# Kernel optimization log

Hardware: AMD Instinct MI355X
Metric: run time of the kernel (lower is better)

## Reference

```python
import jax, jax.numpy as jnp
import numpy as np


def conv2d(x, w, pad, groups=1):
    # x: [B,Cin,H,W], w: [Cout,Cin/groups,K,K]
    return jax.lax.conv_general_dilated(
        x, w, (1, 1), [(pad, pad), (pad, pad)],
        dimension_numbers=('NCHW', 'OIHW', 'NCHW'),
        feature_group_count=groups)


def setup_inputs() -> dict:
    key = jax.random.key(0)
    ks = jax.random.split(key, 24)
    B, C, H, W = 16, 512, 32, 128          # batch, encoder_dim, feature map
    Da, Ds, De, Dm = 512, 256, 256, 1024   # att_dim, state_dim, embed_dim, mem_dim
    V, Dmerge = 1000, 512
    K, P = 11, 5
    Din = De + C + Dm                       # GRU input dim = 1792
    s = 0.02
    rn = lambda k, shp, sc=1.0: jax.random.normal(k, shp, jnp.float32) * sc
    return {
        'encode': rn(ks[0], (B, C, H, W)),
        'encode_pro': rn(ks[1], (B, Da, H, W)),
        'encode_mask': jnp.ones((B, 1, H, W), jnp.float32),
        'state': rn(ks[2], (B, Ds)),
        'pre_weight': jax.random.uniform(ks[3], (B, 1, H, W), jnp.float32),
        'cum_weight': jax.random.uniform(ks[4], (B, 1, H, W), jnp.float32),
        'context': rn(ks[5], (B, C)),
        'cond_mem': rn(ks[6], (B, Dm)),
        'cond_weight': jax.random.uniform(ks[7], (B, 2, H, W), jnp.float32),
        'label_id': jax.random.randint(ks[8], (B,), 0, V),
        # ImageAttention params (all bias-free per source)
        'w_wt': rn(ks[9], (Da, 1, K, K), s),
        'w_cwt': rn(ks[10], (Da, 1, K, K), s),
        'w_condwt': rn(ks[11], (2 * Da, 1, K, K), s),   # groups=2
        'w_energy': rn(ks[12], (Da,), s),               # 1x1 conv -> vector
        'w_state': rn(ks[13], (Da, Ds), s),
        'w_ctx': rn(ks[14], (Da, C), s),
        'w_cond': rn(ks[15], (Da, Dm), s),
        # GRU params
        'w_i2s': rn(ks[16], (Ds, Din), s), 'b_i2s': jnp.zeros((Ds,), jnp.float32),
        'w_i2g': rn(ks[17], (2 * Ds, Din), s), 'b_i2g': jnp.zeros((2 * Ds,), jnp.float32),
        'w_s2g': rn(ks[18], (2 * Ds, Ds), s),
        'w_h2h': rn(ks[19], (Ds, Ds), s),
        # Readout params
        'embed_table': rn(ks[20], (V, De), s),
        'w_l1': rn(ks[21], (Dmerge, De + Ds + C), s), 'b_l1': jnp.zeros((Dmerge,), jnp.float32),
        'w_l2': rn(ks[22], (V, Dmerge), s), 'b_l2': jnp.zeros((V,), jnp.float32),
    }


def reference(encode, encode_pro, encode_mask, state, pre_weight, cum_weight,
              context, cond_mem, cond_weight, label_id, w_wt, w_cwt, w_condwt,
              w_energy, w_state, w_ctx, w_cond, w_i2s, b_i2s, w_i2g, b_i2g,
              w_s2g, w_h2h, embed_table, w_l1, b_l1, w_l2, b_l2):
    P = (w_wt.shape[-1] - 1) // 2
    Da = w_energy.shape[0]
    B, C, H, W = encode.shape
    # --- ImageAttention ---
    t_pre = conv2d(pre_weight, w_wt, P)           # [B,Da,H,W]
    t_cum = conv2d(cum_weight, w_cwt, P)          # [B,Da,H,W]
    t_cw = conv2d(cond_weight, w_condwt, P, groups=2)
    t_cw = t_cw.reshape(B, 2, Da, H, W).sum(1)    # [B,Da,H,W]
    st = state @ w_state.T + context @ w_ctx.T + cond_mem @ w_cond.T  # [B,Da]
    concat_info = jnp.tanh(st[:, :, None, None] + t_pre + t_cum + t_cw + encode_pro)
    energies = jnp.einsum('bchw,c->bhw', concat_info, w_energy)
    energies = energies + (encode_mask[:, 0] - 1.0) * 1e8
    att = jax.nn.softmax(energies.reshape(B, H * W), axis=1)
    new_weight = att.reshape(B, 1, H, W)
    new_cum_weight = cum_weight + new_weight
    ctx = jnp.einsum('bchw,bhw->bc', encode, new_weight[:, 0])  # [B,C]
    # --- GRU transition (data = [embed, ctx, cond_mem]) ---
    embed = embed_table[label_id]
    data = jnp.concatenate([embed, ctx, cond_mem], axis=1)
    gate = data @ w_i2g.T + b_i2g + state @ w_s2g.T
    Ds = state.shape[1]
    update_g = jax.nn.sigmoid(gate[:, :Ds])
    reset_g = jax.nn.sigmoid(gate[:, Ds:])
    state_hat = jnp.tanh(data @ w_i2s.T + b_i2s + (state * reset_g) @ w_h2h.T)
    new_state = update_g * state_hat + (1.0 - update_g) * state
    # --- Readout.step ---
    merged = jnp.concatenate([embed, new_state, ctx], axis=1)
    hid = jax.nn.relu(merged @ w_l1.T + b_l1)
    readout = hid @ w_l2.T + b_l2                  # [B,V]
    return readout
```

## Files before the change

kernel.cpp:

```cpp
#include <hip/hip_runtime.h>
#include <math.h>

typedef unsigned short u16;
typedef __bf16 bf16x8 __attribute__((ext_vector_type(8)));
typedef float f32x4 __attribute__((ext_vector_type(4)));

__device__ u16   g_A_pack[16 * 512 * 32];
__device__ float g_st[16 * 512];
__device__ float g_eraw[16 * 4096];
__device__ float g_energ[16 * 4096];
__device__ float g_data[16 * 1792];
__device__ float g_merged[16 * 1024];
__device__ float g_update[16 * 256];
__device__ float g_reset[16 * 256];
__device__ float g_i2s[16 * 256];
__device__ float g_hid[16 * 512];

__device__ __forceinline__ u16 f2bf(float f) {
    unsigned u = __float_as_uint(f);
    u = (u + 0x7FFFu + ((u >> 16) & 1u)) >> 16;
    return (u16)u;
}
__device__ __forceinline__ float bf2f(u16 u) {
    return __uint_as_float(((unsigned)u) << 16);
}
__device__ __forceinline__ float fast_tanh(float x) {
    return 1.0f - 2.0f / (__expf(2.0f * x) + 1.0f);
}
__device__ __forceinline__ float sigmoidf_(float x) {
    return 1.0f / (1.0f + __expf(-x));
}

__global__ void k_pre(const float* __restrict__ w_wt, const float* __restrict__ w_cwt,
                      const float* __restrict__ w_condwt, const float* __restrict__ state,
                      const float* __restrict__ context, const float* __restrict__ cond_mem,
                      const float* __restrict__ w_state, const float* __restrict__ w_ctx,
                      const float* __restrict__ w_cond, const int* __restrict__ label,
                      const float* __restrict__ embed_table) {
    int bid = blockIdx.x;
    if (bid < 1024) {
        int idx = bid * 256 + threadIdx.x;
        int d = idx >> 9, k = idx & 511;
        float f = 0.f;
        if (k < 484) {
            int c = k / 121, rem = k % 121;
            if (c == 0)      f = w_wt[d * 121 + rem];
            else if (c == 1) f = w_cwt[d * 121 + rem];
            else if (c == 2) f = w_condwt[d * 121 + rem];
            else             f = w_condwt[(512 + d) * 121 + rem];
        }
        int ks = k >> 5, kl = k & 31;
        g_A_pack[(ks * 512 + d) * 32 + kl] = f2bf(f);
    } else if (bid < 3072) {
        int wid = ((bid - 1024) * 256 + threadIdx.x) >> 6;
        int lane = threadIdx.x & 63;
        if (wid >= 16 * 512) return;
        int b = wid >> 9, d = wid & 511;
        float acc = 0.f;
        for (int k = lane; k < 256; k += 64)  acc += state[b * 256 + k]    * w_state[d * 256 + k];
        for (int k = lane; k < 512; k += 64)  acc += context[b * 512 + k]  * w_ctx[d * 512 + k];
        for (int k = lane; k < 1024; k += 64) acc += cond_mem[b * 1024 + k] * w_cond[d * 1024 + k];
        for (int off = 32; off; off >>= 1) acc += __shfl_down(acc, off, 64);
        if (lane == 0) g_st[b * 512 + d] = acc;
    } else {
        int b = bid - 3072, tid = threadIdx.x;
        int lbl = label[b];
        float ev = embed_table[lbl * 256 + tid];
        g_data[b * 1792 + tid] = ev;
        g_merged[b * 1024 + tid] = ev;
        for (int k = tid; k < 1024; k += 256)
            g_data[b * 1792 + 768 + k] = cond_mem[b * 1024 + k];
    }
}

__global__ __launch_bounds__(512, 4) void k_conv_energy(
    const float* __restrict__ pre_w, const float* __restrict__ cum_w, const float* __restrict__ cond_w,
    const float* __restrict__ encode_pro, const float* __restrict__ w_energy)
{
    __shared__ __align__(16) u16 src[4][11][76];
    __shared__ __align__(16) u16 bchunk[64][40];
    __shared__ __align__(16) u16 epro_l[512 * 68];

    const int blk = blockIdx.x;
    const int pxh = blk & 1;
    const int h = (blk >> 1) & 31;
    const int b = blk >> 6;
    const int px0 = pxh * 64;

    const int tid = threadIdx.x;
    const int lane = tid & 63, wv = tid >> 6;
    const int lr = lane & 15, lg = lane >> 4;

    const float* epbase = encode_pro + (size_t)b * 512 * 4096 + h * 128 + px0;

#pragma unroll
    for (int it = 0; it < 7; ++it) {
        int t = tid + it * 512;
        if (t < 4 * 11 * 76) {
            int c = t / (11 * 76);
            int rem = t % (11 * 76);
            int i = rem / 76, x = rem % 76;
            int row = h + i - 5, w = px0 - 5 + x;
            u16 v = 0;
            if (x < 74 && row >= 0 && row < 32 && w >= 0 && w < 128) {
                const float* img = (c == 0) ? pre_w + b * 4096
                                 : (c == 1) ? cum_w + b * 4096
                                 : (c == 2) ? cond_w + b * 8192
                                            : cond_w + b * 8192 + 4096;
                v = f2bf(img[row * 128 + w]);
            }
            src[c][i][x] = v;
        }
    }
    __syncthreads();

    const int kl = tid & 31;
    const int n0 = tid >> 5;
#define BUILD(KS)                                                               \
    {                                                                           \
        int kg = (KS) * 32 + kl;                                                \
        int c = 0, i = 0, jj = 0;                                               \
        bool ok = (kg < 484);                                                   \
        if (ok) { c = kg / 121; int r2 = kg % 121; i = r2 / 11; jj = r2 % 11; } \
        _Pragma("unroll")                                                       \
        for (int rep = 0; rep < 4; ++rep) {                                     \
            int n = n0 + rep * 16;                                              \
            bchunk[n][kl] = ok ? src[c][i][n + jj] : (u16)0;                    \
        }                                                                       \
    }

    f32x4 acc[4][4];
#pragma unroll
    for (int mt = 0; mt < 4; ++mt)
#pragma unroll
        for (int nt = 0; nt < 4; ++nt) {
            f32x4 z = {0.f, 0.f, 0.f, 0.f};
            acc[mt][nt] = z;
        }

    BUILD(0);
    __syncthreads();

#pragma unroll
    for (int ks = 0; ks < 16; ++ks) {
        const int o = ks * 2048 + tid * 4;
        const int er = o >> 6, ec = o & 63;
        float4 epv = *reinterpret_cast<const float4*>(&epbase[(size_t)er * 4096 + ec]);

        bf16x8 afr[4];
#pragma unroll
        for (int mt = 0; mt < 4; ++mt) {
            int d = wv * 64 + mt * 16 + lr;
            afr[mt] = *reinterpret_cast<const bf16x8*>(&g_A_pack[(ks * 512 + d) * 32 + lg * 8]);
        }
        bf16x8 bfr[4];
#pragma unroll
        for (int nt = 0; nt < 4; ++nt)
            bfr[nt] = *reinterpret_cast<const bf16x8*>(&bchunk[nt * 16 + lr][lg * 8]);

#pragma unroll
        for (int mt = 0; mt < 4; ++mt)
#pragma unroll
            for (int nt = 0; nt < 4; ++nt)
                acc[mt][nt] = __builtin_amdgcn_mfma_f32_16x16x32_bf16(afr[mt], bfr[nt], acc[mt][nt], 0, 0, 0);

        {
            ushort4 s;
            s.x = f2bf(epv.x); s.y = f2bf(epv.y); s.z = f2bf(epv.z); s.w = f2bf(epv.w);
            *reinterpret_cast<ushort4*>(&epro_l[er * 68 + ec]) = s;
        }

        __syncthreads();
        if (ks < 15) {
            BUILD(ks + 1);
            __syncthreads();
        }
    }
#undef BUILD

    float e[4] = {0.f, 0.f, 0.f, 0.f};
#pragma unroll
    for (int mt = 0; mt < 4; ++mt) {
#pragma unroll
        for (int r = 0; r < 4; ++r) {
            int d = wv * 64 + mt * 16 + lg * 4 + r;
            float stv = g_st[b * 512 + d];
            float wev = w_energy[d];
#pragma unroll
            for (int nt = 0; nt < 4; ++nt) {
                int px = nt * 16 + lr;
                float val = stv + acc[mt][nt][r] + bf2f(epro_l[d * 68 + px]);
                e[nt] += wev * fast_tanh(val);
            }
        }
    }

    float* ered = reinterpret_cast<float*>(&bchunk[0][0]);
    __syncthreads();
#pragma unroll
    for (int nt = 0; nt < 4; ++nt) {
        float v = e[nt];
        v += __shfl_xor(v, 16, 64);
        v += __shfl_xor(v, 32, 64);
        if (lane < 16) ered[wv * 64 + nt * 16 + lane] = v;
    }
    __syncthreads();
    if (tid < 64) {
        float v = 0.f;
#pragma unroll
        for (int w = 0; w < 8; ++w) v += ered[w * 64 + tid];
        g_eraw[b * 4096 + h * 128 + px0 + tid] = v;
    }
}

__global__ void k_softmax(const float* __restrict__ encode_mask) {
    __shared__ float red[256];
    int b = blockIdx.x, tid = threadIdx.x;
    float v[16];
    float mx = -1e30f;
#pragma unroll
    for (int i = 0; i < 16; ++i) {
        int idx = b * 4096 + tid + i * 256;
        float ev = g_eraw[idx] + (encode_mask[idx] - 1.0f) * 1e8f;
        v[i] = ev; mx = fmaxf(mx, ev);
    }
    red[tid] = mx; __syncthreads();
    for (int s = 128; s; s >>= 1) { if (tid < s) red[tid] = fmaxf(red[tid], red[tid + s]); __syncthreads(); }
    mx = red[0]; __syncthreads();
    float sum = 0.f;
#pragma unroll
    for (int i = 0; i < 16; ++i) { v[i] = __expf(v[i] - mx); sum += v[i]; }
    red[tid] = sum; __syncthreads();
    for (int s = 128; s; s >>= 1) { if (tid < s) red[tid] += red[tid + s]; __syncthreads(); }
    float inv = 1.0f / red[0];
#pragma unroll
    for (int i = 0; i < 16; ++i) g_energ[b * 4096 + tid + i * 256] = v[i] * inv;
}

__global__ void k_ctx(const float* __restrict__ encode) {
    int wid = (blockIdx.x * blockDim.x + threadIdx.x) >> 6;
    int lane = threadIdx.x & 63;
    if (wid >= 16 * 512) return;
    int b = wid >> 9, c = wid & 511;
    const float* e = encode + (size_t)wid * 4096;
    const float* a = g_energ + b * 4096;
    float acc = 0.f;
#pragma unroll
    for (int it = 0; it < 16; ++it) {
        int base = it * 256 + lane * 4;
        float4 ev = *reinterpret_cast<const float4*>(&e[base]);
        float4 av = *reinterpret_cast<const float4*>(&a[base]);
        acc += ev.x * av.x + ev.y * av.y + ev.z * av.z + ev.w * av.w;
    }
    for (int off = 32; off; off >>= 1) acc += __shfl_down(acc, off, 64);
    if (lane == 0) { g_data[b * 1792 + 256 + c] = acc; g_merged[b * 1024 + 512 + c] = acc; }
}

__global__ void k_e1(const float* __restrict__ state,
                     const float* __restrict__ w_i2g, const float* __restrict__ b_i2g,
                     const float* __restrict__ w_s2g, const float* __restrict__ w_i2s,
                     const float* __restrict__ b_i2s) {
    int wid = (blockIdx.x * blockDim.x + threadIdx.x) >> 6;
    int lane = threadIdx.x & 63;
    if (wid >= 16 * 768) return;
    int b = wid / 768, o = wid % 768;
    const float* dt = g_data + b * 1792;
    float acc = 0.f;
    if (o < 512) {
        const float* wr = w_i2g + o * 1792;
        for (int k = lane; k < 1792; k += 64) acc += dt[k] * wr[k];
        const float* wsg = w_s2g + o * 256;
        for (int k = lane; k < 256; k += 64) acc += state[b * 256 + k] * wsg[k];
    } else {
        const float* wr = w_i2s + (o - 512) * 1792;
        for (int k = lane; k < 1792; k += 64) acc += dt[k] * wr[k];
    }
    for (int off = 32; off; off >>= 1) acc += __shfl_down(acc, off, 64);
    if (lane == 0) {
        if (o < 256)       g_update[b * 256 + o]        = sigmoidf_(acc + b_i2g[o]);
        else if (o < 512)  g_reset[b * 256 + (o - 256)] = sigmoidf_(acc + b_i2g[o]);
        else               g_i2s[b * 256 + (o - 512)]   = acc + b_i2s[o - 512];
    }
}

__global__ void k_e2(const float* __restrict__ state, const float* __restrict__ w_h2h) {
    int wid = (blockIdx.x * blockDim.x + threadIdx.x) >> 6;
    int lane = threadIdx.x & 63;
    if (wid >= 16 * 256) return;
    int b = wid >> 8, d = wid & 255;
    const float* wr = w_h2h + d * 256;
    float acc = 0.f;
    for (int k = lane; k < 256; k += 64)
        acc += state[b * 256 + k] * g_reset[b * 256 + k] * wr[k];
    for (int off = 32; off; off >>= 1) acc += __shfl_down(acc, off, 64);
    if (lane == 0) {
        float sh = fast_tanh(g_i2s[b * 256 + d] + acc);
        float u = g_update[b * 256 + d];
        g_merged[b * 1024 + 256 + d] = u * sh + (1.f - u) * state[b * 256 + d];
    }
}

__global__ void k_e3(const float* __restrict__ w_l1, const float* __restrict__ b_l1) {
    int wid = (blockIdx.x * blockDim.x + threadIdx.x) >> 6;
    int lane = threadIdx.x & 63;
    if (wid >= 16 * 512) return;
    int b = wid >> 9, m = wid & 511;
    const float* mg = g_merged + b * 1024;
    const float* wr = w_l1 + m * 1024;
    float acc = 0.f;
    for (int k = lane; k < 1024; k += 64) acc += mg[k] * wr[k];
    for (int off = 32; off; off >>= 1) acc += __shfl_down(acc, off, 64);
    if (lane == 0) g_hid[b * 512 + m] = fmaxf(acc + b_l1[m], 0.f);
}

__global__ void k_e4(const float* __restrict__ w_l2, const float* __restrict__ b_l2,
                     float* __restrict__ out) {
    int wid = (blockIdx.x * blockDim.x + threadIdx.x) >> 6;
    int lane = threadIdx.x & 63;
    if (wid >= 16 * 1000) return;
    int b = wid / 1000, v = wid % 1000;
    const float* hd = g_hid + b * 512;
    const float* wr = w_l2 + v * 512;
    float acc = 0.f;
    for (int k = lane; k < 512; k += 64) acc += hd[k] * wr[k];
    for (int off = 32; off; off >>= 1) acc += __shfl_down(acc, off, 64);
    if (lane == 0) out[b * 1000 + v] = acc + b_l2[v];
}

extern "C" void kernel_launch(void* const* d_in, const int* in_sizes, int n_in,
                              void* d_out, int out_size, void* d_ws, size_t ws_size,
                              hipStream_t stream) {
    static const int EXP[28] = {
        33554432, 33554432, 65536, 4096, 65536, 65536, 8192, 16384, 131072, 16,
        61952, 61952, 123904, 512, 131072, 262144, 524288, 458752, 256, 917504,
        512, 131072, 65536, 256000, 524288, 512, 512000, 1000};
    if (n_in != 28) return;
    for (int i = 0; i < 28; ++i)
        if (in_sizes[i] != EXP[i]) return;

    const float* encode      = (const float*)d_in[0];
    const float* encode_pro  = (const float*)d_in[1];
    const float* encode_mask = (const float*)d_in[2];
    const float* state       = (const float*)d_in[3];
    const float* pre_weight  = (const float*)d_in[4];
    const float* cum_weight  = (const float*)d_in[5];
    const float* context     = (const float*)d_in[6];
    const float* cond_mem    = (const float*)d_in[7];
    const float* cond_weight = (const float*)d_in[8];
    const int*   label_id    = (const int*)d_in[9];
    const float* w_wt     = (const float*)d_in[10];
    const float* w_cwt    = (const float*)d_in[11];
    const float* w_condwt = (const float*)d_in[12];
    const float* w_energy = (const float*)d_in[13];
    const float* w_state  = (const float*)d_in[14];
    const float* w_ctx    = (const float*)d_in[15];
    const float* w_cond   = (const float*)d_in[16];
    const float* w_i2s    = (const float*)d_in[17];
    const float* b_i2s    = (const float*)d_in[18];
    const float* w_i2g    = (const float*)d_in[19];
    const float* b_i2g    = (const float*)d_in[20];
    const float* w_s2g    = (const float*)d_in[21];
    const float* w_h2h    = (const float*)d_in[22];
    const float* embed_t  = (const float*)d_in[23];
    const float* w_l1     = (const float*)d_in[24];
    const float* b_l1     = (const float*)d_in[25];
    const float* w_l2     = (const float*)d_in[26];
    const float* b_l2     = (const float*)d_in[27];
    float* out = (float*)d_out;
    (void)d_ws; (void)ws_size;

    k_pre<<<3088, 256, 0, stream>>>(w_wt, w_cwt, w_condwt, state, context, cond_mem,
                                    w_state, w_ctx, w_cond, label_id, embed_t);
    k_conv_energy<<<1024, 512, 0, stream>>>(pre_weight, cum_weight, cond_weight,
                                            encode_pro, w_energy);
    k_softmax<<<16, 256, 0, stream>>>(encode_mask);
    k_ctx<<<2048, 256, 0, stream>>>(encode);
    k_e1<<<3072, 256, 0, stream>>>(state, w_i2g, b_i2g, w_s2g, w_i2s, b_i2s);
    k_e2<<<1024, 256, 0, stream>>>(state, w_h2h);
    k_e3<<<2048, 256, 0, stream>>>(w_l1, b_l1);
    k_e4<<<4000, 256, 0, stream>>>(w_l2, b_l2, out);
}
```

Baseline: 178.8 us.

## Fuse softmax into context kernel and hoist encode_pro staging before MFMA loop

Two changes. The per-batch softmax is folded into the context-reduction kernel: each of 512 blocks recomputes its batch's softmax into shared memory and then reduces 16 channels against it. This removes a kernel launch and the global round trip of the attention weights, at the cost of computing the softmax redundantly 32 times per batch. Separately, the conv-energy kernel now loads and bf16-converts the whole encode_pro tile up front instead of interleaving those loads with the MFMA k-loop, and that loop is no longer unrolled, which may reduce load/compute overlap.

```diff
diff --git a/kernel.cpp b/kernel.cpp
--- a/kernel.cpp
+++ b/kernel.cpp
@@ -8,7 +8,6 @@
 __device__ u16   g_A_pack[16 * 512 * 32];
 __device__ float g_st[16 * 512];
 __device__ float g_eraw[16 * 4096];
-__device__ float g_energ[16 * 4096];
 __device__ float g_data[16 * 1792];
 __device__ float g_merged[16 * 1024];
 __device__ float g_update[16 * 256];
@@ -91,7 +90,18 @@
     const int lane = tid & 63, wv = tid >> 6;
     const int lr = lane & 15, lg = lane >> 4;
 
-    const float* epbase = encode_pro + (size_t)b * 512 * 4096 + h * 128 + px0;
+    {
+        const float* epbase = encode_pro + (size_t)b * 512 * 4096 + h * 128 + px0;
+#pragma unroll
+        for (int i = 0; i < 16; ++i) {
+            int o = i * 2048 + tid * 4;
+            int r = o >> 6, c = o & 63;
+            float4 v = *reinterpret_cast<const float4*>(&epbase[(size_t)r * 4096 + c]);
+            ushort4 s;
+            s.x = f2bf(v.x); s.y = f2bf(v.y); s.z = f2bf(v.z); s.w = f2bf(v.w);
+            *reinterpret_cast<ushort4*>(&epro_l[r * 68 + c]) = s;
+        }
+    }
 
 #pragma unroll
     for (int it = 0; it < 7; ++it) {
@@ -141,12 +151,7 @@
     BUILD(0);
     __syncthreads();
 
-#pragma unroll
     for (int ks = 0; ks < 16; ++ks) {
-        const int o = ks * 2048 + tid * 4;
-        const int er = o >> 6, ec = o & 63;
-        float4 epv = *reinterpret_cast<const float4*>(&epbase[(size_t)er * 4096 + ec]);
-
         bf16x8 afr[4];
 #pragma unroll
         for (int mt = 0; mt < 4; ++mt) {
@@ -163,13 +168,6 @@
 #pragma unroll
             for (int nt = 0; nt < 4; ++nt)
                 acc[mt][nt] = __builtin_amdgcn_mfma_f32_16x16x32_bf16(afr[mt], bfr[nt], acc[mt][nt], 0, 0, 0);
-
-        {
-            ushort4 s;
-            s.x = f2bf(epv.x); s.y = f2bf(epv.y); s.z = f2bf(epv.z); s.w = f2bf(epv.w);
-            *reinterpret_cast<ushort4*>(&epro_l[er * 68 + ec]) = s;
-        }
-
         __syncthreads();
         if (ks < 15) {
             BUILD(ks + 1);
@@ -213,15 +211,23 @@
     }
 }
 
-__global__ void k_softmax(const float* __restrict__ encode_mask) {
+__global__ __launch_bounds__(256) void k_ctx(const float* __restrict__ encode,
+                                             const float* __restrict__ encode_mask) {
+    __shared__ float att[4096];
     __shared__ float red[256];
-    int b = blockIdx.x, tid = threadIdx.x;
+
+    const int bid = blockIdx.x;
+    const int b = bid >> 5;
+    const int c0 = (bid & 31) * 16;
+    const int tid = threadIdx.x;
+    const int lane = tid & 63, wvi = tid >> 6;
+
     float v[16];
     float mx = -1e30f;
 #pragma unroll
     for (int i = 0; i < 16; ++i) {
-        int idx = b * 4096 + tid + i * 256;
-        float ev = g_eraw[idx] + (encode_mask[idx] - 1.0f) * 1e8f;
+        int idx = tid + i * 256;
+        float ev = g_eraw[b * 4096 + idx] + (encode_mask[b * 4096 + idx] - 1.0f) * 1e8f;
         v[i] = ev; mx = fmaxf(mx, ev);
     }
     red[tid] = mx; __syncthreads();
@@ -234,26 +240,24 @@
     for (int s = 128; s; s >>= 1) { if (tid < s) red[tid] += red[tid + s]; __syncthreads(); }
     float inv = 1.0f / red[0];
 #pragma unroll
-    for (int i = 0; i < 16; ++i) g_energ[b * 4096 + tid + i * 256] = v[i] * inv;
-}
-
-__global__ void k_ctx(const float* __restrict__ encode) {
-    int wid = (blockIdx.x * blockDim.x + threadIdx.x) >> 6;
-    int lane = threadIdx.x & 63;
-    if (wid >= 16 * 512) return;
-    int b = wid >> 9, c = wid & 511;
-    const float* e = encode + (size_t)wid * 4096;
-    const float* a = g_energ + b * 4096;
-    float acc = 0.f;
-#pragma unroll
-    for (int it = 0; it < 16; ++it) {
-        int base = it * 256 + lane * 4;
-        float4 ev = *reinterpret_cast<const float4*>(&e[base]);
-        float4 av = *reinterpret_cast<const float4*>(&a[base]);
-        acc += ev.x * av.x + ev.y * av.y + ev.z * av.z + ev.w * av.w;
-    }
-    for (int off = 32; off; off >>= 1) acc += __shfl_down(acc, off, 64);
-    if (lane == 0) { g_data[b * 1792 + 256 + c] = acc; g_merged[b * 1024 + 512 + c] = acc; }
+    for (int i = 0; i < 16; ++i) att[tid + i * 256] = v[i] * inv;
+    __syncthreads();
+
+#pragma unroll
+    for (int cc = 0; cc < 4; ++cc) {
+        int c = c0 + wvi * 4 + cc;
+        const float* e = encode + ((size_t)b * 512 + c) * 4096;
+        float acc = 0.f;
+#pragma unroll
+        for (int it = 0; it < 16; ++it) {
+            int base = it * 256 + lane * 4;
+            float4 ev = *reinterpret_cast<const float4*>(&e[base]);
+            float4 av = *reinterpret_cast<const float4*>(&att[base]);
+            acc += ev.x * av.x + ev.y * av.y + ev.z * av.z + ev.w * av.w;
+        }
+        for (int off = 32; off; off >>= 1) acc += __shfl_down(acc, off, 64);
+        if (lane == 0) { g_data[b * 1792 + 256 + c] = acc; g_merged[b * 1024 + 512 + c] = acc; }
+    }
 }
 
 __global__ void k_e1(const float* __restrict__ state,
@@ -373,8 +377,7 @@
                                     w_state, w_ctx, w_cond, label_id, embed_t);
     k_conv_energy<<<1024, 512, 0, stream>>>(pre_weight, cum_weight, cond_weight,
                                             encode_pro, w_energy);
-    k_softmax<<<16, 256, 0, stream>>>(encode_mask);
-    k_ctx<<<2048, 256, 0, stream>>>(encode);
+    k_ctx<<<512, 256, 0, stream>>>(encode, encode_mask);
     k_e1<<<3072, 256, 0, stream>>>(state, w_i2g, b_i2g, w_s2g, w_i2s, b_i2s);
     k_e2<<<1024, 256, 0, stream>>>(state, w_h2h);
     k_e3<<<2048, 256, 0, stream>>>(w_l1, b_l1);
```

Result: faster. 161.2 us (median of 2 runs) (-9.8%).
